# Kernel optimization log

Measured on AMD Instinct MI355X. Metric: run time of the kernel, lower is better.

Reference implementation:

```python
import jax, jax.numpy as jnp
import numpy as np

B, T, C = 4, 2048, 1024
H = 16
D = C // H  # head_dim = 64


def setup_inputs() -> dict:
    key = jax.random.key(0)
    k1, k2, k3 = jax.random.split(key, 3)
    x = jax.random.normal(k1, (B, T, C), dtype=jnp.float32)
    w_qkv = jax.random.normal(k2, (C, 3 * C), dtype=jnp.float32) * (C ** -0.5)
    b_qkv = jnp.zeros((3 * C,), dtype=jnp.float32)
    w_proj = jax.random.normal(k3, (C, C), dtype=jnp.float32) * (C ** -0.5)
    b_proj = jnp.zeros((C,), dtype=jnp.float32)
    return {"x": x, "w_qkv": w_qkv, "b_qkv": b_qkv, "w_proj": w_proj, "b_proj": b_proj}


def reference(x, w_qkv, b_qkv, w_proj, b_proj):
    # qkv projection: (B,T,C) -> (B,T,3,H,D) -> q,k,v each (B,H,T,D)
    qkv = (x @ w_qkv + b_qkv).reshape(B, T, 3, H, D)
    q, k, v = jnp.moveaxis(qkv, 2, 0)           # each (B, T, H, D)
    q = q.transpose(0, 2, 1, 3)                 # (B, H, T, D)
    k = k.transpose(0, 2, 1, 3)
    v = v.transpose(0, 2, 1, 3)

    scale = 1.0 / jnp.sqrt(jnp.float32(D))
    attn = jnp.einsum('bhqd,bhkd->bhqk', q, k) * scale  # (B,H,T,T)
    causal = jnp.tril(jnp.ones((T, T), dtype=bool))
    attn = jnp.where(causal[None, None], attn, -jnp.inf)
    attn = jax.nn.softmax(attn, axis=-1)
    # dropout p=0.0 (eval mode) -> identity
    out = jnp.einsum('bhqk,bhkd->bhqd', attn, v)        # (B,H,T,D)
    out = out.transpose(0, 2, 1, 3).reshape(B, T, C)
    return out @ w_proj + b_proj
```

## Files before the change

kernel.cpp:

```cpp
#include <hip/hip_runtime.h>
#include <hip/hip_bf16.h>


#define Bsz 4
#define Tsz 2048
#define Csz 1024
#define Hn  16
#define Dh  64

typedef unsigned short u16;
typedef __attribute__((ext_vector_type(8))) short bf16x8;
typedef __attribute__((ext_vector_type(4))) float f32x4;
typedef __attribute__((ext_vector_type(4))) unsigned int u32x4;
typedef __attribute__((ext_vector_type(2))) unsigned int u32x2;

__device__ __forceinline__ u16 f2b(float f) {
  __hip_bfloat16 h = __float2bfloat16(f);
  return *reinterpret_cast<u16*>(&h);
}

__device__ __forceinline__ unsigned pk2(float lo, float hi) {
  return (unsigned)f2b(lo) | ((unsigned)f2b(hi) << 16);
}

__device__ __forceinline__ void gld_lds16(const void* g, void* lds) {
  __builtin_amdgcn_global_load_lds(
      (const __attribute__((address_space(1))) unsigned int*)g,
      (__attribute__((address_space(3))) unsigned int*)lds, 16, 0, 0);
}

__global__ __launch_bounds__(256) void cvt_f32_bf16(const float* __restrict__ in,
                                                    u16* __restrict__ out) {
  size_t i = ((size_t)blockIdx.x * 256 + threadIdx.x) * 8;
  f32x4 a = *(const f32x4*)(in + i);
  f32x4 b = *(const f32x4*)(in + i + 4);
  u16 r[8];
#pragma unroll
  for (int j = 0; j < 4; ++j) { r[j] = f2b(a[j]); r[4 + j] = f2b(b[j]); }
  *(u32x4*)(out + i) = *(const u32x4*)r;
}

__global__ __launch_bounds__(256) void cvt_transpose(const float* __restrict__ in,
                                                     u16* __restrict__ out,
                                                     int R, int C) {
  __shared__ u16 tile[64 * 66];
  const int r0 = blockIdx.x * 64, c0 = blockIdx.y * 64;
  const int tid = threadIdx.x;
#pragma unroll
  for (int i = 0; i < 16; ++i) {
    int idx = i * 256 + tid;
    int r = idx >> 6, c = idx & 63;
    tile[r * 66 + c] = f2b(in[(size_t)(r0 + r) * C + (c0 + c)]);
  }
  __syncthreads();
#pragma unroll
  for (int i = 0; i < 16; ++i) {
    int idx = i * 256 + tid;
    int c = idx >> 6, r = idx & 63;
    out[(size_t)(c0 + c) * R + (r0 + r)] = tile[r * 66 + c];
  }
}

__device__ __forceinline__ void gemm_tile_acc(const u16* __restrict__ A,
                                              const u16* __restrict__ Bt,
                                              int m0, int n0,
                                              u16* Alds, u16* Blds,
                                              f32x4 acc[4][4]) {
  const int tid = threadIdx.x;
  const int w = tid >> 6, lane = tid & 63;
  const int wm = w & 1, wn = w >> 1;
  const int col = lane & 15, quad = lane >> 4;
  const int lrow = lane >> 2;
  const int kseg = (lane & 3) * 8;
#pragma unroll
  for (int mt = 0; mt < 4; ++mt)
#pragma unroll
    for (int nt = 0; nt < 4; ++nt)
      acc[mt][nt] = (f32x4){0.f, 0.f, 0.f, 0.f};

  for (int k0 = 0; k0 < 1024; k0 += 32) {
    __syncthreads();
#pragma unroll
    for (int g = 0; g < 2; ++g) {
      int grp = w * 2 + g;
      gld_lds16(A + (size_t)(m0 + grp * 16 + lrow) * 1024 + k0 + kseg,
                (char*)Alds + grp * 1024);
      gld_lds16(Bt + (size_t)(n0 + grp * 16 + lrow) * 1024 + k0 + kseg,
                (char*)Blds + grp * 1024);
    }
    __syncthreads();
    bf16x8 af[4], bfr[4];
#pragma unroll
    for (int mt = 0; mt < 4; ++mt)
      af[mt] = *(const bf16x8*)(Alds + (wm * 64 + mt * 16 + col) * 32 + quad * 8);
#pragma unroll
    for (int nt = 0; nt < 4; ++nt)
      bfr[nt] = *(const bf16x8*)(Blds + (wn * 64 + nt * 16 + col) * 32 + quad * 8);
#pragma unroll
    for (int mt = 0; mt < 4; ++mt)
#pragma unroll
      for (int nt = 0; nt < 4; ++nt)
        acc[mt][nt] = __builtin_amdgcn_mfma_f32_16x16x32_bf16(af[mt], bfr[nt],
                                                              acc[mt][nt], 0, 0, 0);
  }
}

__global__ __launch_bounds__(256) void gemm_qkv(const u16* __restrict__ X,
                                                const u16* __restrict__ WT,
                                                const float* __restrict__ bias,
                                                u16* __restrict__ Q,
                                                u16* __restrict__ Kc,
                                                u16* __restrict__ Vt) {
  __shared__ __align__(16) u16 Alds[128 * 32];
  __shared__ __align__(16) u16 Blds[128 * 32];
  f32x4 acc[4][4];
  const int m0 = blockIdx.x * 128, n0 = blockIdx.y * 128;
  gemm_tile_acc(X, WT, m0, n0, Alds, Blds, acc);

  const float qscale = 0.18033688011112042f;
  const int tid = threadIdx.x;
  const int w = tid >> 6, lane = tid & 63;
  const int wm = w & 1, wn = w >> 1;
  const int col = lane & 15, quad = lane >> 4;
#pragma unroll
  for (int mt = 0; mt < 4; ++mt)
#pragma unroll
    for (int nt = 0; nt < 4; ++nt) {
      int n = n0 + wn * 64 + nt * 16 + col;
      int s = n >> 10, hh = (n >> 6) & (Hn - 1), d = n & 63;
      int mBase = m0 + wm * 64 + mt * 16 + quad * 4;
      int b = mBase >> 11, t0 = mBase & (Tsz - 1);
      if (s == 2) {
        u16 vals[4];
#pragma unroll
        for (int r = 0; r < 4; ++r) vals[r] = f2b(acc[mt][nt][r] + bias[n]);
        *(u32x2*)(Vt + ((size_t)(b * Hn + hh) * Dh + d) * Tsz + t0) =
            *(const u32x2*)vals;
      } else {
        const float scl = (s == 0) ? qscale : 1.f;
        u16* dst = (s == 0) ? Q : Kc;
#pragma unroll
        for (int r = 0; r < 4; ++r)
          dst[((size_t)(b * Hn + hh) * Tsz + (t0 + r)) * Dh + d] =
              f2b((acc[mt][nt][r] + bias[n]) * scl);
      }
    }
}

__global__ __launch_bounds__(256) void gemm_proj(const u16* __restrict__ O,
                                                 const u16* __restrict__ WT,
                                                 const float* __restrict__ bias,
                                                 float* __restrict__ out) {
  __shared__ __align__(16) u16 Alds[128 * 32];
  __shared__ __align__(16) u16 Blds[128 * 32];
  f32x4 acc[4][4];
  const int m0 = blockIdx.x * 128, n0 = blockIdx.y * 128;
  gemm_tile_acc(O, WT, m0, n0, Alds, Blds, acc);

  const int tid = threadIdx.x;
  const int w = tid >> 6, lane = tid & 63;
  const int wm = w & 1, wn = w >> 1;
  const int col = lane & 15, quad = lane >> 4;
#pragma unroll
  for (int mt = 0; mt < 4; ++mt)
#pragma unroll
    for (int nt = 0; nt < 4; ++nt)
#pragma unroll
      for (int r = 0; r < 4; ++r) {
        int m = m0 + wm * 64 + mt * 16 + quad * 4 + r;
        int n = n0 + wn * 64 + nt * 16 + col;
        out[(size_t)m * Csz + n] = acc[mt][nt][r] + bias[n];
      }
}

__global__ __launch_bounds__(512, 6) void attn(const u16* __restrict__ Q,
                                               const u16* __restrict__ Kg,
                                               const u16* __restrict__ Vt,
                                               u16* __restrict__ O) {
  __shared__ __align__(16) u16 Ks[2][64 * 64];
  __shared__ __align__(16) u16 Vs[2][64 * 64];

  const int d0 = blockIdx.x + (blockIdx.y << 4) + (blockIdx.z << 8);
  const int xcd = d0 & 7;
  const int l = d0 >> 3;
  const int r0_ = l >> 5, c0_ = l & 31;
  const int a_ = c0_ >> 1, p_ = c0_ & 1;
  const int qt = (r0_ & 1) ? a_ : (15 - a_);
  const int bh = (((p_ << 2) | r0_) << 3) | xcd;
  const int h = bh & (Hn - 1), b = bh >> 4;

  const int tid = threadIdx.x, w = tid >> 6, lane = tid & 63;
  const int col = lane & 15, quad = lane >> 4;
  const int qbase = qt << 7;

  const u16* Kbase = Kg + (size_t)bh * Tsz * Dh;
  const u16* Vbase = Vt + (size_t)bh * Dh * Tsz;

  const int trow = tid >> 3;
  const int xseg = ((tid & 7) ^ (trow & 7)) * 8;
  const size_t koff = (size_t)trow * 64 + xseg;
  const size_t voff = (size_t)trow * Tsz + xseg;
  const int swz = col & 7;
  const int off0 = ((0 + quad) ^ swz) << 3;
  const int off1 = ((4 + quad) ^ swz) << 3;

  const int nst = 2 * qt + 2;
  gld_lds16(Kbase + koff, &Ks[0][w * 512]);
  gld_lds16(Vbase + voff, &Vs[0][w * 512]);

  const u16* Qg = Q + ((size_t)bh * Tsz + qbase) * Dh;
  bf16x8 aq[2];
#pragma unroll
  for (int ks = 0; ks < 2; ++ks)
    aq[ks] = *(const bf16x8*)(Qg + (size_t)(w * 16 + col) * Dh + ks * 32 + quad * 8);
  asm volatile("s_waitcnt vmcnt(0)" ::: "memory");

  f32x4 oacc[4];
#pragma unroll
  for (int dt = 0; dt < 4; ++dt) oacc[dt] = (f32x4){0.f, 0.f, 0.f, 0.f};
  float lsum[4] = {0.f, 0.f, 0.f, 0.f};

  const u16* kdma = Kbase + 4096 + koff;
  const u16* vdma = Vbase + 64 + voff;

  const int qg = w * 16 + col;
  const int smask = 2 * qt + (w >= 4 ? 1 : 0);

  for (int s = 0; s < nst; ++s) {
    asm volatile("s_waitcnt vmcnt(0)" ::: "memory");
    __builtin_amdgcn_s_barrier();
    __builtin_amdgcn_sched_barrier(0);
    const int cur = s & 1;
    if (s + 1 < nst) {
      const int nxt = cur ^ 1;
      gld_lds16(kdma, &Ks[nxt][w * 512]);
      gld_lds16(vdma, &Vs[nxt][w * 512]);
      kdma += 4096;
      vdma += 64;
    }

    if (w >= 4 || s < nst - 1) {
      f32x4 sacc[4];
#pragma unroll
      for (int kt = 0; kt < 4; ++kt) sacc[kt] = (f32x4){0.f, 0.f, 0.f, 0.f};
#pragma unroll
      for (int ks = 0; ks < 2; ++ks)
#pragma unroll
        for (int kt = 0; kt < 4; ++kt) {
          bf16x8 bk = *(const bf16x8*)(
              &Ks[cur][(kt * 16 + col) * 64 + (ks ? off1 : off0)]);
          sacc[kt] = __builtin_amdgcn_mfma_f32_16x16x32_bf16(bk, aq[ks],
                                                             sacc[kt], 0, 0, 0);
        }

      float e[4][4];
      if (s >= smask) {
        const int rel = (s - 2 * qt) << 6;
#pragma unroll
        for (int kt = 0; kt < 4; ++kt)
#pragma unroll
          for (int r = 0; r < 4; ++r) {
            int kl = rel + kt * 16 + quad * 4 + r;
            float p = (kl > qg) ? 0.f : exp2f(sacc[kt][r]);
            lsum[kt] += p;
            e[kt][r] = p;
          }
      } else {
#pragma unroll
        for (int kt = 0; kt < 4; ++kt)
#pragma unroll
          for (int r = 0; r < 4; ++r) {
            float p = exp2f(sacc[kt][r]);
            lsum[kt] += p;
            e[kt][r] = p;
          }
      }

#pragma unroll
      for (int ksg = 0; ksg < 2; ++ksg) {
        unsigned w00 = pk2(e[2 * ksg][0], e[2 * ksg][1]);
        unsigned w01 = pk2(e[2 * ksg][2], e[2 * ksg][3]);
        unsigned w10 = pk2(e[2 * ksg + 1][0], e[2 * ksg + 1][1]);
        unsigned w11 = pk2(e[2 * ksg + 1][2], e[2 * ksg + 1][3]);
        auto ra = __builtin_amdgcn_permlane32_swap(w00, w10, false, false);
        auto rb = __builtin_amdgcn_permlane32_swap(w01, w11, false, false);
        auto sa = __builtin_amdgcn_permlane16_swap(ra[0], ra[1], false, false);
        auto sb = __builtin_amdgcn_permlane16_swap(rb[0], rb[1], false, false);
        union { unsigned u[4]; bf16x8 v; } pf;
        pf.u[0] = sa[0]; pf.u[1] = sb[0]; pf.u[2] = sa[1]; pf.u[3] = sb[1];
#pragma unroll
        for (int dt = 0; dt < 4; ++dt) {
          bf16x8 bv = *(const bf16x8*)(
              &Vs[cur][(dt * 16 + col) * 64 + (ksg ? off1 : off0)]);
          oacc[dt] = __builtin_amdgcn_mfma_f32_16x16x32_bf16(bv, pf.v,
                                                             oacc[dt], 0, 0, 0);
        }
      }
    }
  }

  float v = (lsum[0] + lsum[1]) + (lsum[2] + lsum[3]);
  v += __shfl_xor(v, 16);
  v += __shfl_xor(v, 32);
  const float inv = 1.0f / v;

  const int rg = qbase + w * 16 + col;
  u16* Orow = O + (((size_t)b * Tsz + rg) * Hn + h) * Dh;
#pragma unroll
  for (int dt = 0; dt < 4; ++dt) {
    u16 vals[4];
#pragma unroll
    for (int r = 0; r < 4; ++r) vals[r] = f2b(oacc[dt][r] * inv);
    *(u32x2*)(Orow + dt * 16 + quad * 4) = *(const u32x2*)vals;
  }
}

extern "C" void kernel_launch(void* const* d_in, const int* in_sizes, int n_in,
                              void* d_out, int out_size, void* d_ws, size_t ws_size,
                              hipStream_t stream) {
  const float* x      = (const float*)d_in[0];
  const float* w_qkv  = (const float*)d_in[1];
  const float* b_qkv  = (const float*)d_in[2];
  const float* w_proj = (const float*)d_in[3];
  const float* b_proj = (const float*)d_in[4];
  float* out = (float*)d_out;

  u16* Xb     = (u16*)d_ws;
  u16* WqkvT  = Xb + (size_t)8192 * 1024;
  u16* WprojT = WqkvT + (size_t)3072 * 1024;
  u16* Qb     = WprojT + (size_t)1024 * 1024;
  u16* Kb     = Qb + (size_t)8192 * 1024;
  u16* Ob     = Kb + (size_t)8192 * 1024;
  u16* Vtb    = (u16*)d_out;

  cvt_f32_bf16<<<4096, 256, 0, stream>>>(x, Xb);
  cvt_transpose<<<dim3(16, 48), 256, 0, stream>>>(w_qkv, WqkvT, 1024, 3072);
  cvt_transpose<<<dim3(16, 16), 256, 0, stream>>>(w_proj, WprojT, 1024, 1024);
  gemm_qkv<<<dim3(64, 24), 256, 0, stream>>>(Xb, WqkvT, b_qkv, Qb, Kb, Vtb);
  attn<<<dim3(16, 16, 4), 512, 0, stream>>>(Qb, Kb, Vtb, Ob);
  gemm_proj<<<dim3(64, 8), 256, 0, stream>>>(Ob, WprojT, b_proj, out);
}
```

Measured before the change: 274.3 us.

## Pair low and high causal query tiles per block to share K/V loads

Each attention block now processes two query tiles (qt and 15-qt) of the same head, reusing each staged K/V tile for both, and the grid shrinks from 1024 to 512 blocks. This balances causal work per block and halves the K/V global-to-LDS traffic for the low tile. In exchange it doubles the accumulator registers, lowers the occupancy hint from 6 to 4, and gives fewer blocks to spread across CUs.

```diff
diff --git a/kernel.cpp b/kernel.cpp
--- a/kernel.cpp
+++ b/kernel.cpp
@@ -173,25 +173,83 @@
       }
 }
 
-__global__ __launch_bounds__(512, 6) void attn(const u16* __restrict__ Q,
+__device__ __forceinline__ void attn_tile_stage(
+    const u16* __restrict__ Kc, const u16* __restrict__ Vc,
+    const bf16x8* aq, f32x4* oacc, float* lsum,
+    bool domask, int rel, int qg, int col, int quad, int off0, int off1) {
+  f32x4 sacc[4];
+#pragma unroll
+  for (int kt = 0; kt < 4; ++kt) sacc[kt] = (f32x4){0.f, 0.f, 0.f, 0.f};
+#pragma unroll
+  for (int ks = 0; ks < 2; ++ks)
+#pragma unroll
+    for (int kt = 0; kt < 4; ++kt) {
+      bf16x8 bk = *(const bf16x8*)(&Kc[(kt * 16 + col) * 64 + (ks ? off1 : off0)]);
+      sacc[kt] = __builtin_amdgcn_mfma_f32_16x16x32_bf16(bk, aq[ks],
+                                                         sacc[kt], 0, 0, 0);
+    }
+
+  float e[4][4];
+  if (domask) {
+#pragma unroll
+    for (int kt = 0; kt < 4; ++kt)
+#pragma unroll
+      for (int r = 0; r < 4; ++r) {
+        int kl = rel + kt * 16 + quad * 4 + r;
+        float p = (kl > qg) ? 0.f : exp2f(sacc[kt][r]);
+        lsum[kt] += p;
+        e[kt][r] = p;
+      }
+  } else {
+#pragma unroll
+    for (int kt = 0; kt < 4; ++kt)
+#pragma unroll
+      for (int r = 0; r < 4; ++r) {
+        float p = exp2f(sacc[kt][r]);
+        lsum[kt] += p;
+        e[kt][r] = p;
+      }
+  }
+
+#pragma unroll
+  for (int ksg = 0; ksg < 2; ++ksg) {
+    unsigned w00 = pk2(e[2 * ksg][0], e[2 * ksg][1]);
+    unsigned w01 = pk2(e[2 * ksg][2], e[2 * ksg][3]);
+    unsigned w10 = pk2(e[2 * ksg + 1][0], e[2 * ksg + 1][1]);
+    unsigned w11 = pk2(e[2 * ksg + 1][2], e[2 * ksg + 1][3]);
+    auto ra = __builtin_amdgcn_permlane32_swap(w00, w10, false, false);
+    auto rb = __builtin_amdgcn_permlane32_swap(w01, w11, false, false);
+    auto sa = __builtin_amdgcn_permlane16_swap(ra[0], ra[1], false, false);
+    auto sb = __builtin_amdgcn_permlane16_swap(rb[0], rb[1], false, false);
+    union { unsigned u[4]; bf16x8 v; } pf;
+    pf.u[0] = sa[0]; pf.u[1] = sb[0]; pf.u[2] = sa[1]; pf.u[3] = sb[1];
+#pragma unroll
+    for (int dt = 0; dt < 4; ++dt) {
+      bf16x8 bv = *(const bf16x8*)(&Vc[(dt * 16 + col) * 64 + (ksg ? off1 : off0)]);
+      oacc[dt] = __builtin_amdgcn_mfma_f32_16x16x32_bf16(bv, pf.v,
+                                                         oacc[dt], 0, 0, 0);
+    }
+  }
+}
+
+__global__ __launch_bounds__(512, 4) void attn(const u16* __restrict__ Q,
                                                const u16* __restrict__ Kg,
                                                const u16* __restrict__ Vt,
                                                u16* __restrict__ O) {
   __shared__ __align__(16) u16 Ks[2][64 * 64];
   __shared__ __align__(16) u16 Vs[2][64 * 64];
 
-  const int d0 = blockIdx.x + (blockIdx.y << 4) + (blockIdx.z << 8);
+  const int d0 = blockIdx.x;
   const int xcd = d0 & 7;
-  const int l = d0 >> 3;
-  const int r0_ = l >> 5, c0_ = l & 31;
-  const int a_ = c0_ >> 1, p_ = c0_ & 1;
-  const int qt = (r0_ & 1) ? a_ : (15 - a_);
-  const int bh = (((p_ << 2) | r0_) << 3) | xcd;
+  const int idx = d0 >> 3;
+  const int bh = ((idx & 7) << 3) | xcd;
+  const int a = idx >> 3;
+  const int qlo = a, qhi = 15 - a;
   const int h = bh & (Hn - 1), b = bh >> 4;
 
   const int tid = threadIdx.x, w = tid >> 6, lane = tid & 63;
   const int col = lane & 15, quad = lane >> 4;
-  const int qbase = qt << 7;
+  const int qbl = qlo << 7, qbh = qhi << 7;
 
   const u16* Kbase = Kg + (size_t)bh * Tsz * Dh;
   const u16* Vbase = Vt + (size_t)bh * Dh * Tsz;
@@ -204,27 +262,40 @@
   const int off0 = ((0 + quad) ^ swz) << 3;
   const int off1 = ((4 + quad) ^ swz) << 3;
 
-  const int nst = 2 * qt + 2;
+  const int nst = 2 * qhi + 2;
   gld_lds16(Kbase + koff, &Ks[0][w * 512]);
   gld_lds16(Vbase + voff, &Vs[0][w * 512]);
 
-  const u16* Qg = Q + ((size_t)bh * Tsz + qbase) * Dh;
-  bf16x8 aq[2];
-#pragma unroll
-  for (int ks = 0; ks < 2; ++ks)
-    aq[ks] = *(const bf16x8*)(Qg + (size_t)(w * 16 + col) * Dh + ks * 32 + quad * 8);
+  bf16x8 aq_hi[2], aq_lo[2];
+  {
+    const u16* Qh = Q + ((size_t)bh * Tsz + qbh) * Dh;
+    const u16* Ql = Q + ((size_t)bh * Tsz + qbl) * Dh;
+#pragma unroll
+    for (int ks = 0; ks < 2; ++ks) {
+      aq_hi[ks] = *(const bf16x8*)(Qh + (size_t)(w * 16 + col) * Dh + ks * 32 + quad * 8);
+      aq_lo[ks] = *(const bf16x8*)(Ql + (size_t)(w * 16 + col) * Dh + ks * 32 + quad * 8);
+    }
+  }
   asm volatile("s_waitcnt vmcnt(0)" ::: "memory");
 
-  f32x4 oacc[4];
-#pragma unroll
-  for (int dt = 0; dt < 4; ++dt) oacc[dt] = (f32x4){0.f, 0.f, 0.f, 0.f};
-  float lsum[4] = {0.f, 0.f, 0.f, 0.f};
+  f32x4 oacc_hi[4], oacc_lo[4];
+#pragma unroll
+  for (int dt = 0; dt < 4; ++dt) {
+    oacc_hi[dt] = (f32x4){0.f, 0.f, 0.f, 0.f};
+    oacc_lo[dt] = (f32x4){0.f, 0.f, 0.f, 0.f};
+  }
+  float lsum_hi[4] = {0.f, 0.f, 0.f, 0.f};
+  float lsum_lo[4] = {0.f, 0.f, 0.f, 0.f};
 
   const u16* kdma = Kbase + 4096 + koff;
   const u16* vdma = Vbase + 64 + voff;
 
   const int qg = w * 16 + col;
-  const int smask = 2 * qt + (w >= 4 ? 1 : 0);
+  const int wge4 = (w >= 4) ? 1 : 0;
+  const int smask_hi = 2 * qhi + wge4;
+  const int smask_lo = 2 * qlo + wge4;
+  const int lo_end = 2 * qlo + 1 + wge4;
+  const int hi2 = 2 * qhi, lo2 = 2 * qlo;
 
   for (int s = 0; s < nst; ++s) {
     asm volatile("s_waitcnt vmcnt(0)" ::: "memory");
@@ -238,80 +309,40 @@
       kdma += 4096;
       vdma += 64;
     }
-
-    if (w >= 4 || s < nst - 1) {
-      f32x4 sacc[4];
-#pragma unroll
-      for (int kt = 0; kt < 4; ++kt) sacc[kt] = (f32x4){0.f, 0.f, 0.f, 0.f};
-#pragma unroll
-      for (int ks = 0; ks < 2; ++ks)
-#pragma unroll
-        for (int kt = 0; kt < 4; ++kt) {
-          bf16x8 bk = *(const bf16x8*)(
-              &Ks[cur][(kt * 16 + col) * 64 + (ks ? off1 : off0)]);
-          sacc[kt] = __builtin_amdgcn_mfma_f32_16x16x32_bf16(bk, aq[ks],
-                                                             sacc[kt], 0, 0, 0);
-        }
-
-      float e[4][4];
-      if (s >= smask) {
-        const int rel = (s - 2 * qt) << 6;
-#pragma unroll
-        for (int kt = 0; kt < 4; ++kt)
-#pragma unroll
-          for (int r = 0; r < 4; ++r) {
-            int kl = rel + kt * 16 + quad * 4 + r;
-            float p = (kl > qg) ? 0.f : exp2f(sacc[kt][r]);
-            lsum[kt] += p;
-            e[kt][r] = p;
-          }
-      } else {
-#pragma unroll
-        for (int kt = 0; kt < 4; ++kt)
-#pragma unroll
-          for (int r = 0; r < 4; ++r) {
-            float p = exp2f(sacc[kt][r]);
-            lsum[kt] += p;
-            e[kt][r] = p;
-          }
-      }
-
-#pragma unroll
-      for (int ksg = 0; ksg < 2; ++ksg) {
-        unsigned w00 = pk2(e[2 * ksg][0], e[2 * ksg][1]);
-        unsigned w01 = pk2(e[2 * ksg][2], e[2 * ksg][3]);
-        unsigned w10 = pk2(e[2 * ksg + 1][0], e[2 * ksg + 1][1]);
-        unsigned w11 = pk2(e[2 * ksg + 1][2], e[2 * ksg + 1][3]);
-        auto ra = __builtin_amdgcn_permlane32_swap(w00, w10, false, false);
-        auto rb = __builtin_amdgcn_permlane32_swap(w01, w11, false, false);
-        auto sa = __builtin_amdgcn_permlane16_swap(ra[0], ra[1], false, false);
-        auto sb = __builtin_amdgcn_permlane16_swap(rb[0], rb[1], false, false);
-        union { unsigned u[4]; bf16x8 v; } pf;
-        pf.u[0] = sa[0]; pf.u[1] = sb[0]; pf.u[2] = sa[1]; pf.u[3] = sb[1];
-#pragma unroll
-        for (int dt = 0; dt < 4; ++dt) {
-          bf16x8 bv = *(const bf16x8*)(
-              &Vs[cur][(dt * 16 + col) * 64 + (ksg ? off1 : off0)]);
-          oacc[dt] = __builtin_amdgcn_mfma_f32_16x16x32_bf16(bv, pf.v,
-                                                             oacc[dt], 0, 0, 0);
-        }
-      }
-    }
-  }
-
-  float v = (lsum[0] + lsum[1]) + (lsum[2] + lsum[3]);
-  v += __shfl_xor(v, 16);
-  v += __shfl_xor(v, 32);
-  const float inv = 1.0f / v;
-
-  const int rg = qbase + w * 16 + col;
-  u16* Orow = O + (((size_t)b * Tsz + rg) * Hn + h) * Dh;
+    const u16* Kc = &Ks[cur][0];
+    const u16* Vc = &Vs[cur][0];
+
+    if (w >= 4 || s < nst - 1)
+      attn_tile_stage(Kc, Vc, aq_hi, oacc_hi, lsum_hi,
+                      s >= smask_hi, (s - hi2) * 64, qg, col, quad, off0, off1);
+    if (s < lo_end)
+      attn_tile_stage(Kc, Vc, aq_lo, oacc_lo, lsum_lo,
+                      s >= smask_lo, (s - lo2) * 64, qg, col, quad, off0, off1);
+  }
+
+  float vh = (lsum_hi[0] + lsum_hi[1]) + (lsum_hi[2] + lsum_hi[3]);
+  vh += __shfl_xor(vh, 16);
+  vh += __shfl_xor(vh, 32);
+  const float invh = 1.0f / vh;
+  float vl = (lsum_lo[0] + lsum_lo[1]) + (lsum_lo[2] + lsum_lo[3]);
+  vl += __shfl_xor(vl, 16);
+  vl += __shfl_xor(vl, 32);
+  const float invl = 1.0f / vl;
+
+  const int rgh = qbh + w * 16 + col;
+  const int rgl = qbl + w * 16 + col;
+  u16* OrowH = O + (((size_t)b * Tsz + rgh) * Hn + h) * Dh;
+  u16* OrowL = O + (((size_t)b * Tsz + rgl) * Hn + h) * Dh;
 #pragma unroll
   for (int dt = 0; dt < 4; ++dt) {
-    u16 vals[4];
-#pragma unroll
-    for (int r = 0; r < 4; ++r) vals[r] = f2b(oacc[dt][r] * inv);
-    *(u32x2*)(Orow + dt * 16 + quad * 4) = *(const u32x2*)vals;
+    u16 vh4[4], vl4[4];
+#pragma unroll
+    for (int r = 0; r < 4; ++r) {
+      vh4[r] = f2b(oacc_hi[dt][r] * invh);
+      vl4[r] = f2b(oacc_lo[dt][r] * invl);
+    }
+    *(u32x2*)(OrowH + dt * 16 + quad * 4) = *(const u32x2*)vh4;
+    *(u32x2*)(OrowL + dt * 16 + quad * 4) = *(const u32x2*)vl4;
   }
 }
 
@@ -337,6 +368,6 @@
   cvt_transpose<<<dim3(16, 48), 256, 0, stream>>>(w_qkv, WqkvT, 1024, 3072);
   cvt_transpose<<<dim3(16, 16), 256, 0, stream>>>(w_proj, WprojT, 1024, 1024);
   gemm_qkv<<<dim3(64, 24), 256, 0, stream>>>(Xb, WqkvT, b_qkv, Qb, Kb, Vtb);
-  attn<<<dim3(16, 16, 4), 512, 0, stream>>>(Qb, Kb, Vtb, Ob);
+  attn<<<dim3(512), 512, 0, stream>>>(Qb, Kb, Vtb, Ob);
   gemm_proj<<<dim3(64, 8), 256, 0, stream>>>(Ob, WprojT, b_proj, out);
 }
```

Result: faster. 255.5 us (-6.8%).
